# Kernel tuning notes

Hardware: AMD Instinct MI355X
Metric: run time of the kernel (lower is better)

The kernel has to match this reference:

```python
import jax, jax.numpy as jnp
import numpy as np

IN_DIM = 1024
EMBED = 1024
HEADS = 16
HEAD_DIM = EMBED // HEADS
MAX_LEN = 401


def _sinusoidal_pe(max_len, d_model):
    pos = np.arange(max_len, dtype=np.float32)[:, None]
    div = np.exp(np.arange(0, d_model, 2, dtype=np.float32) * (-np.log(10000.0) / d_model))
    pe = np.zeros((max_len, d_model), dtype=np.float32)
    pe[:, 0::2] = np.sin(pos * div)
    pe[:, 1::2] = np.cos(pos * div)
    return jnp.asarray(pe[None])  # [1, max_len, d]


def setup_inputs() -> dict:
    key = jax.random.key(0)
    ks = jax.random.split(key, 16)
    B, S = 32, 400
    s = 1.0 / np.sqrt(IN_DIM)
    inp = {
        "query": jax.random.normal(ks[0], (B, S, IN_DIM), jnp.float32),
        "key": jax.random.normal(ks[1], (B, S, IN_DIM), jnp.float32),
        "value": jax.random.normal(ks[2], (B, S, IN_DIM), jnp.float32),
        "attn_mask": jnp.zeros((S, S), jnp.float32),
        "pe": _sinusoidal_pe(MAX_LEN, IN_DIM),
        "Wq": jax.random.normal(ks[3], (EMBED, IN_DIM), jnp.float32) * s,
        "bq": jax.random.normal(ks[4], (EMBED,), jnp.float32) * s,
        "Wk": jax.random.normal(ks[5], (EMBED, IN_DIM), jnp.float32) * s,
        "bk": jax.random.normal(ks[6], (EMBED,), jnp.float32) * s,
        "Wv": jax.random.normal(ks[7], (EMBED, IN_DIM), jnp.float32) * s,
        "bv": jax.random.normal(ks[8], (EMBED,), jnp.float32) * s,
        "Wp": jax.random.normal(ks[9], (EMBED, IN_DIM), jnp.float32) * s,
        "bp": jax.random.normal(ks[10], (EMBED,), jnp.float32) * s,
        "Wo": jax.random.normal(ks[11], (IN_DIM, EMBED), jnp.float32) / np.sqrt(EMBED),
        "bo": jax.random.normal(ks[12], (IN_DIM,), jnp.float32) / np.sqrt(EMBED),
        "gates": jax.random.normal(ks[13], (1,), jnp.float32),
    }
    return inp


def reference(query, key, value, attn_mask, pe, Wq, bq, Wk, bk, Wv, bv, Wp, bp, Wo, bo, gates):
    B, Sq, _ = query.shape
    Sk = key.shape[1]
    H, D = HEADS, HEAD_DIM

    pos_q = pe[:, :Sq] @ Wp.T + bp   # [1, Sq, E]
    pos_k = pe[:, :Sk] @ Wp.T + bp   # [1, Sk, E]

    q = (query @ Wq.T + bq + pos_q).reshape(B, Sq, H, D).transpose(0, 2, 1, 3)
    k = (key @ Wk.T + bk + pos_k).reshape(B, Sk, H, D).transpose(0, 2, 1, 3)
    v = (value @ Wv.T + bv + pos_k).reshape(B, Sk, H, D).transpose(0, 2, 1, 3)

    scores = jnp.einsum('bhqd,bhkd->bhqk', q, k) / jnp.sqrt(jnp.float32(D))
    scores = scores + attn_mask[None, None]  # additive mask broadcast over batch/heads
    attn = jax.nn.softmax(scores, axis=-1)   # dropout p=0.0 -> identity

    out = jnp.einsum('bhqk,bhkd->bhqd', attn, v)
    out = out.transpose(0, 2, 1, 3).reshape(B, Sq, H * D)
    return (out @ Wo.T + bo) * gates
```

## Files before the change

### kernel.cpp

```cpp
#include <hip/hip_runtime.h>

typedef __bf16 bf16;
typedef __bf16 bf16x8 __attribute__((ext_vector_type(8)));
typedef __bf16 bf16x4 __attribute__((ext_vector_type(4)));
typedef float f32x4 __attribute__((ext_vector_type(4)));

#define MFMA(a, b, c) __builtin_amdgcn_mfma_f32_16x16x32_bf16(a, b, c, 0, 0, 0)

__device__ __forceinline__ void g2l16(void* lds, const void* g) {
  __builtin_amdgcn_global_load_lds(
      (const __attribute__((address_space(1))) void*)g,
      (__attribute__((address_space(3))) void*)lds, 16, 0, 0);
}

__global__ void cvt_all(
    const float* __restrict__ Wq, const float* __restrict__ Wk, const float* __restrict__ Wv,
    const float* __restrict__ Wo, const float* __restrict__ Wp, const float* __restrict__ pe,
    const float* __restrict__ Xq, const float* __restrict__ Xk, const float* __restrict__ Xv,
    bf16* __restrict__ wqb, bf16* __restrict__ wkb, bf16* __restrict__ wvb,
    bf16* __restrict__ wob, bf16* __restrict__ wpb, bf16* __restrict__ peb,
    bf16* __restrict__ xqb, bf16* __restrict__ xkb, bf16* __restrict__ xvb) {
  int b = blockIdx.x;
  const float* s;
  bf16* d;
  int lb;
  if (b < 5120) {
    int t = b >> 10;
    lb = b & 1023;
    s = (t == 0) ? Wq : (t == 1) ? Wk : (t == 2) ? Wv : (t == 3) ? Wo : Wp;
    d = (t == 0) ? wqb : (t == 1) ? wkb : (t == 2) ? wvb : (t == 3) ? wob : wpb;
  } else if (b < 5520) {
    lb = b - 5120;
    s = pe;
    d = peb;
  } else {
    int bb = b - 5520;
    int t = bb / 12800;
    lb = bb - t * 12800;
    s = (t == 0) ? Xq : (t == 1) ? Xk : Xv;
    d = (t == 0) ? xqb : (t == 1) ? xkb : xvb;
  }
  int i = lb * 256 + threadIdx.x;
  f32x4 v = *(const f32x4*)(s + (size_t)i * 4);
  bf16x4 o;
  o[0] = (bf16)v[0]; o[1] = (bf16)v[1]; o[2] = (bf16)v[2]; o[3] = (bf16)v[3];
  *(bf16x4*)(d + (size_t)i * 4) = o;
}

__global__ __launch_bounds__(256) void gemm_pos(
    const bf16* __restrict__ peb, const bf16* __restrict__ Wpb,
    const float* __restrict__ bp, const float* __restrict__ bq,
    const float* __restrict__ bk, const float* __restrict__ bv,
    bf16* __restrict__ posq, bf16* __restrict__ posk, bf16* __restrict__ posv) {
  __shared__ bf16 smA[128 * 32];
  __shared__ bf16 smB[128 * 32];
  const int mbase = blockIdx.y * 128;
  const int nbase = blockIdx.x * 128;
  const int tid = threadIdx.x;
  const int lane = tid & 63, w = tid >> 6;
  const int wm = (w >> 1) * 64, wn = (w & 1) * 64;
  const int lrow = lane & 15, kg = lane >> 4;
  const f32x4 fz = {0.f, 0.f, 0.f, 0.f};
  f32x4 acc[4][4];
#pragma unroll
  for (int i = 0; i < 4; ++i)
#pragma unroll
    for (int j = 0; j < 4; ++j) acc[i][j] = fz;

  for (int k0 = 0; k0 < 1024; k0 += 32) {
    __syncthreads();
#pragma unroll
    for (int it = 0; it < 2; ++it) {
      int j = it * 256 + tid;
      int r = j >> 2, cl = j & 3;
      int c = cl ^ ((r >> 1) & 3);
      if (mbase + r < 400)
        g2l16(smA + j * 8, peb + (mbase + r) * 1024 + k0 + c * 8);
      else {
        uint4 zz = make_uint4(0, 0, 0, 0);
        *(uint4*)(smA + j * 8) = zz;
      }
    }
#pragma unroll
    for (int it = 0; it < 2; ++it) {
      int j = it * 256 + tid;
      int r = j >> 2, cl = j & 3;
      int c = cl ^ ((r >> 1) & 3);
      g2l16(smB + j * 8, Wpb + (nbase + r) * 1024 + k0 + c * 8);
    }
    __syncthreads();
    bf16x8 af[4], bfr[4];
#pragma unroll
    for (int mt = 0; mt < 4; ++mt) {
      int r = wm + mt * 16 + lrow;
      int ch = kg ^ ((r >> 1) & 3);
      af[mt] = *(const bf16x8*)(smA + r * 32 + ch * 8);
    }
#pragma unroll
    for (int nt = 0; nt < 4; ++nt) {
      int r = wn + nt * 16 + lrow;
      int ch = kg ^ ((r >> 1) & 3);
      bfr[nt] = *(const bf16x8*)(smB + r * 32 + ch * 8);
    }
#pragma unroll
    for (int nt = 0; nt < 4; ++nt)
#pragma unroll
      for (int mt = 0; mt < 4; ++mt)
        acc[mt][nt] = MFMA(af[mt], bfr[nt], acc[mt][nt]);
  }
#pragma unroll
  for (int mt = 0; mt < 4; ++mt)
#pragma unroll
    for (int rg = 0; rg < 4; ++rg) {
      int m = mbase + wm + mt * 16 + kg * 4 + rg;
      if (m < 400) {
#pragma unroll
        for (int nt = 0; nt < 4; ++nt) {
          int n = nbase + wn + nt * 16 + lrow;
          float base = acc[mt][nt][rg] + bp[n];
          posq[m * 1024 + n] = (bf16)(base + bq[n]);
          posk[m * 1024 + n] = (bf16)(base + bk[n]);
          posv[m * 1024 + n] = (bf16)(base + bv[n]);
        }
      }
    }
}

__global__ __launch_bounds__(512, 4) void gemm_qkv(
    const bf16* __restrict__ Xqb, const bf16* __restrict__ Xkb, const bf16* __restrict__ Xvb,
    const bf16* __restrict__ Wqb, const bf16* __restrict__ Wkb, const bf16* __restrict__ Wvb,
    const bf16* __restrict__ posq, const bf16* __restrict__ posk, const bf16* __restrict__ posv,
    bf16* __restrict__ qb, bf16* __restrict__ kbuf, bf16* __restrict__ vt) {
  const int lid = blockIdx.x;
  const int mI = ((lid >> 6) << 3) + (lid & 7);
  const int nI = (lid >> 3) & 7;
  if (mI >= 100) return;
  __shared__ bf16 sm[16384];
  bf16* smA = sm;
  bf16* smB = sm + 8192;
  const int z = blockIdx.y;
  const bf16* X = (z == 0) ? Xqb : (z == 1) ? Xkb : Xvb;
  const bf16* W = (z == 0) ? Wqb : (z == 1) ? Wkb : Wvb;
  const bf16* posz = (z == 0) ? posq : (z == 1) ? posk : posv;
  const int mbase = mI * 128;
  const int nbase = nI * 128;
  const int tid = threadIdx.x;
  const int lane = tid & 63, w = tid >> 6;
  const int wm = (w >> 1) * 32, wn = (w & 1) * 64;
  const int lrow = lane & 15, kg = lane >> 4;
  const f32x4 fz = {0.f, 0.f, 0.f, 0.f};
  f32x4 acc[2][4];
#pragma unroll
  for (int i = 0; i < 2; ++i)
#pragma unroll
    for (int j = 0; j < 4; ++j) acc[i][j] = fz;

  for (int k0 = 0; k0 < 1024; k0 += 64) {
    __syncthreads();
#pragma unroll
    for (int it = 0; it < 2; ++it) {
      int j = it * 512 + tid;
      int r = j >> 3, cl = j & 7;
      g2l16(smA + j * 8, X + (size_t)(mbase + r) * 1024 + k0 + (cl ^ (r & 7)) * 8);
    }
#pragma unroll
    for (int it = 0; it < 2; ++it) {
      int j = it * 512 + tid;
      int r = j >> 3, cl = j & 7;
      g2l16(smB + j * 8, W + (size_t)(nbase + r) * 1024 + k0 + (cl ^ (r & 7)) * 8);
    }
    __syncthreads();
#pragma unroll
    for (int ks = 0; ks < 2; ++ks) {
      bf16x8 af[2], bfr[4];
#pragma unroll
      for (int mt = 0; mt < 2; ++mt) {
        int r = wm + mt * 16 + lrow;
        af[mt] = *(const bf16x8*)(smA + r * 64 + ((ks * 4 + kg) ^ (r & 7)) * 8);
      }
#pragma unroll
      for (int nt = 0; nt < 4; ++nt) {
        int r = wn + nt * 16 + lrow;
        bfr[nt] = *(const bf16x8*)(smB + r * 64 + ((ks * 4 + kg) ^ (r & 7)) * 8);
      }
#pragma unroll
      for (int nt = 0; nt < 4; ++nt)
#pragma unroll
        for (int mt = 0; mt < 2; ++mt)
          acc[mt][nt] = MFMA(af[mt], bfr[nt], acc[mt][nt]);
    }
  }

  if (z < 2) {
    bf16* dst = (z == 0) ? qb : kbuf;
#pragma unroll
    for (int mt = 0; mt < 2; ++mt)
#pragma unroll
      for (int rg = 0; rg < 4; ++rg) {
        int m = mbase + wm + mt * 16 + kg * 4 + rg;
        int bI = m / 400;
        int s = m - bI * 400;
#pragma unroll
        for (int nt = 0; nt < 4; ++nt) {
          int n = nbase + wn + nt * 16 + lrow;
          float v = acc[mt][nt][rg] + (float)posz[s * 1024 + n];
          int h = n >> 6, d = n & 63;
          dst[((size_t)(bI * 16 + h) * 400 + s) * 64 + d] = (bf16)v;
        }
      }
  } else {
    __syncthreads();
    bf16* T = sm;
#pragma unroll
    for (int nt = 0; nt < 4; ++nt) {
      int n = wn + nt * 16 + lrow;
      int ng = nbase + n;
#pragma unroll
      for (int mt = 0; mt < 2; ++mt) {
        int m0 = wm + mt * 16 + kg * 4;
        bf16x4 v4;
#pragma unroll
        for (int rg = 0; rg < 4; ++rg) {
          int m = mbase + m0 + rg;
          int bI = m / 400;
          int s = m - bI * 400;
          v4[rg] = (bf16)(acc[mt][nt][rg] + (float)posz[s * 1024 + ng]);
        }
        int chk = m0 >> 3;
        int st = chk ^ (n & 15);
        *(bf16x4*)(T + n * 128 + st * 8 + (m0 & 7)) = v4;
      }
    }
    __syncthreads();
#pragma unroll
    for (int p = 0; p < 4; ++p) {
      int n = p * 32 + (tid >> 4);
      int chk = tid & 15;
      bf16x8 row = *(const bf16x8*)(T + n * 128 + (chk ^ (n & 15)) * 8);
      int ng = nbase + n;
      int h = ng >> 6, d = ng & 63;
      int m = mbase + chk * 8;
      int bI = m / 400;
      int s = m - bI * 400;
      *(bf16x8*)(vt + ((size_t)(bI * 16 + h) * 64 + d) * 400 + s) = row;
    }
  }
}

__global__ __launch_bounds__(512, 4) void attn_kernel(
    const bf16* __restrict__ qg, const bf16* __restrict__ kg_,
    const bf16* __restrict__ vg, const float* __restrict__ mask,
    bf16* __restrict__ ao) {
  const int lid = blockIdx.x;
  const int qt = (lid >> 3) & 3;
  const int bh = ((lid >> 5) << 3) + (lid & 7);
  __shared__ bf16 smQ[128 * 64];
  __shared__ bf16 smK[128 * 64];
  __shared__ bf16 smV[64 * 128];
  __shared__ bf16 smP[128 * 128];
  const int qbase = qt * 128;
  const int tid = threadIdx.x;
  const int lane = tid & 63;
  const int w = tid >> 6;
  const int lrow = lane & 15, kg = lane >> 4;
  const bf16* Qg = qg + bh * 25600;
  const bf16* Kg = kg_ + bh * 25600;
  const bf16* Vg = vg + bh * 25600;

#pragma unroll
  for (int it = 0; it < 2; ++it) {
    int j = it * 512 + tid;
    int r = j >> 3, cl = j & 7;
    int c = cl ^ (r & 7);
    int s = qbase + r;
    uint4 val = make_uint4(0, 0, 0, 0);
    if (s < 400) val = *(const uint4*)(Qg + s * 64 + c * 8);
    *(uint4*)(smQ + j * 8) = val;
  }

  const f32x4 fz = {0.f, 0.f, 0.f, 0.f};
  f32x4 o[4];
#pragma unroll
  for (int i = 0; i < 4; ++i) o[i] = fz;
  float m_run[4], l_run[4];
#pragma unroll
  for (int i = 0; i < 4; ++i) { m_run[i] = -1e30f; l_run[i] = 0.f; }

  for (int kt = 0; kt < 4; ++kt) {
#pragma unroll
    for (int it = 0; it < 2; ++it) {
      int j = it * 512 + tid;
      int r = j >> 3, cl = j & 7;
      int c = cl ^ (r & 7);
      int s = kt * 128 + r;
      uint4 val = make_uint4(0, 0, 0, 0);
      if (s < 400) val = *(const uint4*)(Kg + s * 64 + c * 8);
      *(uint4*)(smK + j * 8) = val;
    }
#pragma unroll
    for (int it = 0; it < 2; ++it) {
      int j = it * 512 + tid;
      int r = j >> 4, cl = j & 15;
      int c = cl ^ (r & 15);
      int s0 = kt * 128 + c * 8;
      uint4 val = make_uint4(0, 0, 0, 0);
      if (s0 < 400) val = *(const uint4*)(Vg + r * 400 + s0);
      *(uint4*)(smV + j * 8) = val;
    }
    __syncthreads();

    f32x4 sc[8];
#pragma unroll
    for (int nt = 0; nt < 8; ++nt) sc[nt] = fz;
#pragma unroll
    for (int ks = 0; ks < 2; ++ks) {
      int rq = w * 16 + lrow;
      int chq = (ks * 4 + kg) ^ (rq & 7);
      bf16x8 aq = *(const bf16x8*)(smQ + rq * 64 + chq * 8);
#pragma unroll
      for (int nt = 0; nt < 8; ++nt) {
        int rk = nt * 16 + lrow;
        int chk = (ks * 4 + kg) ^ (rk & 7);
        bf16x8 bk8 = *(const bf16x8*)(smK + rk * 64 + chk * 8);
        sc[nt] = MFMA(aq, bk8, sc[nt]);
      }
    }
    float alpha[4];
#pragma unroll
    for (int rg = 0; rg < 4; ++rg) {
      int qs = qbase + w * 16 + kg * 4 + rg;
      float rmax = -1e30f;
#pragma unroll
      for (int nt = 0; nt < 8; ++nt) {
        int ksi = kt * 128 + nt * 16 + lrow;
        float v = sc[nt][rg] * 0.125f;
        v += (ksi < 400) ? ((qs < 400) ? mask[qs * 400 + ksi] : 0.f) : -1e30f;
        sc[nt][rg] = v;
        rmax = fmaxf(rmax, v);
      }
#pragma unroll
      for (int off = 1; off < 16; off <<= 1)
        rmax = fmaxf(rmax, __shfl_xor(rmax, off, 64));
      float mn = fmaxf(m_run[rg], rmax);
      alpha[rg] = __expf(m_run[rg] - mn);
      m_run[rg] = mn;
      float rsum = 0.f;
#pragma unroll
      for (int nt = 0; nt < 8; ++nt) {
        float p = __expf(sc[nt][rg] - mn);
        sc[nt][rg] = p;
        rsum += p;
      }
#pragma unroll
      for (int off = 1; off < 16; off <<= 1)
        rsum += __shfl_xor(rsum, off, 64);
      l_run[rg] = l_run[rg] * alpha[rg] + rsum;
    }
#pragma unroll
    for (int nt2 = 0; nt2 < 4; ++nt2)
#pragma unroll
      for (int rg = 0; rg < 4; ++rg) o[nt2][rg] *= alpha[rg];
#pragma unroll
    for (int nt = 0; nt < 8; ++nt)
#pragma unroll
      for (int rg = 0; rg < 4; ++rg) {
        int row = w * 16 + kg * 4 + rg;
        int col = nt * 16 + lrow;
        int ch = (col >> 3) ^ (row & 15);
        smP[row * 128 + ch * 8 + (col & 7)] = (bf16)sc[nt][rg];
      }
    __syncthreads();
#pragma unroll
    for (int ks2 = 0; ks2 < 4; ++ks2) {
      int rp = w * 16 + lrow;
      int chp = (ks2 * 4 + kg) ^ (rp & 15);
      bf16x8 ap = *(const bf16x8*)(smP + rp * 128 + chp * 8);
#pragma unroll
      for (int nt2 = 0; nt2 < 4; ++nt2) {
        int rv = nt2 * 16 + lrow;
        int chv = (ks2 * 4 + kg) ^ (rv & 15);
        bf16x8 bv8 = *(const bf16x8*)(smV + rv * 128 + chv * 8);
        o[nt2] = MFMA(ap, bv8, o[nt2]);
      }
    }
    __syncthreads();
  }
  const int b = bh >> 4, h = bh & 15;
#pragma unroll
  for (int rg = 0; rg < 4; ++rg) {
    int qs = qbase + w * 16 + kg * 4 + rg;
    if (qs < 400) {
      float inv = 1.f / l_run[rg];
#pragma unroll
      for (int nt2 = 0; nt2 < 4; ++nt2) {
        ao[(b * 400 + qs) * 1024 + h * 64 + nt2 * 16 + lrow] =
            (bf16)(o[nt2][rg] * inv);
      }
    }
  }
}

__global__ __launch_bounds__(512, 4) void gemm_out(
    const bf16* __restrict__ aop, const bf16* __restrict__ Wob,
    const float* __restrict__ bo, const float* __restrict__ gates,
    float* __restrict__ out) {
  const int lid = blockIdx.x;
  const int mI = ((lid >> 6) << 3) + (lid & 7);
  const int nI = (lid >> 3) & 7;
  if (mI >= 100) return;
  __shared__ bf16 sm[16384];
  bf16* smA = sm;
  bf16* smB = sm + 8192;
  const int mbase = mI * 128;
  const int nbase = nI * 128;
  const int tid = threadIdx.x;
  const int lane = tid & 63, w = tid >> 6;
  const int wm = (w >> 1) * 32, wn = (w & 1) * 64;
  const int lrow = lane & 15, kg = lane >> 4;
  const float g = gates[0];
  const f32x4 fz = {0.f, 0.f, 0.f, 0.f};
  f32x4 acc[2][4];
#pragma unroll
  for (int i = 0; i < 2; ++i)
#pragma unroll
    for (int j = 0; j < 4; ++j) acc[i][j] = fz;

  for (int k0 = 0; k0 < 1024; k0 += 64) {
    __syncthreads();
#pragma unroll
    for (int it = 0; it < 2; ++it) {
      int j = it * 512 + tid;
      int r = j >> 3, cl = j & 7;
      g2l16(smA + j * 8, aop + (size_t)(mbase + r) * 1024 + k0 + (cl ^ (r & 7)) * 8);
    }
#pragma unroll
    for (int it = 0; it < 2; ++it) {
      int j = it * 512 + tid;
      int r = j >> 3, cl = j & 7;
      g2l16(smB + j * 8, Wob + (size_t)(nbase + r) * 1024 + k0 + (cl ^ (r & 7)) * 8);
    }
    __syncthreads();
#pragma unroll
    for (int ks = 0; ks < 2; ++ks) {
      bf16x8 af[2], bfr[4];
#pragma unroll
      for (int mt = 0; mt < 2; ++mt) {
        int r = wm + mt * 16 + lrow;
        af[mt] = *(const bf16x8*)(smA + r * 64 + ((ks * 4 + kg) ^ (r & 7)) * 8);
      }
#pragma unroll
      for (int nt = 0; nt < 4; ++nt) {
        int r = wn + nt * 16 + lrow;
        bfr[nt] = *(const bf16x8*)(smB + r * 64 + ((ks * 4 + kg) ^ (r & 7)) * 8);
      }
#pragma unroll
      for (int nt = 0; nt < 4; ++nt)
#pragma unroll
        for (int mt = 0; mt < 2; ++mt)
          acc[mt][nt] = MFMA(af[mt], bfr[nt], acc[mt][nt]);
    }
  }
#pragma unroll
  for (int mt = 0; mt < 2; ++mt)
#pragma unroll
    for (int rg = 0; rg < 4; ++rg) {
      int m = mbase + wm + mt * 16 + kg * 4 + rg;
#pragma unroll
      for (int nt = 0; nt < 4; ++nt) {
        int n = nbase + wn + nt * 16 + lrow;
        out[(size_t)m * 1024 + n] = (acc[mt][nt][rg] + bo[n]) * g;
      }
    }
}

extern "C" void kernel_launch(void* const* d_in, const int* in_sizes, int n_in,
                              void* d_out, int out_size, void* d_ws, size_t ws_size,
                              hipStream_t stream) {
  const float* query = (const float*)d_in[0];
  const float* key   = (const float*)d_in[1];
  const float* value = (const float*)d_in[2];
  const float* mask  = (const float*)d_in[3];
  const float* pe    = (const float*)d_in[4];
  const float* Wq = (const float*)d_in[5];
  const float* bq = (const float*)d_in[6];
  const float* Wk = (const float*)d_in[7];
  const float* bk = (const float*)d_in[8];
  const float* Wv = (const float*)d_in[9];
  const float* bv = (const float*)d_in[10];
  const float* Wp = (const float*)d_in[11];
  const float* bp = (const float*)d_in[12];
  const float* Wo = (const float*)d_in[13];
  const float* bo = (const float*)d_in[14];
  const float* gates = (const float*)d_in[15];
  float* out = (float*)d_out;

  char* base = (char*)d_ws;
  size_t off = 0;
  bf16* wq_b = (bf16*)(base + off); off += 2097152;
  bf16* wk_b = (bf16*)(base + off); off += 2097152;
  bf16* wv_b = (bf16*)(base + off); off += 2097152;
  bf16* wo_b = (bf16*)(base + off); off += 2097152;
  bf16* wp_b = (bf16*)(base + off); off += 2097152;
  bf16* pe_b = (bf16*)(base + off); off += 819200;
  bf16* posq = (bf16*)(base + off); off += 819200;
  bf16* posk = (bf16*)(base + off); off += 819200;
  bf16* posv = (bf16*)(base + off); off += 819200;
  bf16* qb = (bf16*)(base + off); off += 26214400;
  bf16* kb = (bf16*)(base + off); off += 26214400;
  bf16* vt = (bf16*)(base + off); off += 26214400;
  bf16* ao = (bf16*)(base + off); off += 26214400;
  bf16* xq_b = ao;
  bf16* xk_b = (bf16*)d_out;
  bf16* xv_b = (bf16*)d_out + 13107200;
  (void)ws_size; (void)in_sizes; (void)n_in; (void)out_size;

  cvt_all<<<43920, 256, 0, stream>>>(Wq, Wk, Wv, Wo, Wp, pe,
                                     query, key, value,
                                     wq_b, wk_b, wv_b, wo_b, wp_b, pe_b,
                                     xq_b, xk_b, xv_b);
  gemm_pos<<<dim3(8, 4), 256, 0, stream>>>(pe_b, wp_b, bp, bq, bk, bv,
                                           posq, posk, posv);
  gemm_qkv<<<dim3(832, 3), 512, 0, stream>>>(xq_b, xk_b, xv_b,
                                             wq_b, wk_b, wv_b,
                                             posq, posk, posv, qb, kb, vt);
  attn_kernel<<<2048, 512, 0, stream>>>(qb, kb, vt, mask, ao);
  gemm_out<<<832, 512, 0, stream>>>(ao, wo_b, bo, gates, out);
}
```

Before: 524.1 us.

## Prefetch next K/V tile into registers and raise MFMA wave priority in attention

The attention kernel now loads the next key/value tile from global memory into registers while the current tile is being computed, then writes it to LDS at the start of the next iteration. This hides global load latency behind the QK and softmax work. It also wraps the MFMA loops with s_setprio and splits the mask/bounds handling so full tiles skip the per-element bounds checks, using an fma for scale plus mask. The cost is extra register pressure from holding the prefetched tiles, which could lower occupancy.

```diff
diff --git a/kernel.cpp b/kernel.cpp
--- a/kernel.cpp
+++ b/kernel.cpp
@@ -278,6 +278,22 @@
     *(uint4*)(smQ + j * 8) = val;
   }
 
+  uint4 rk[2], rv[2];
+#pragma unroll
+  for (int it = 0; it < 2; ++it) {
+    int j = it * 512 + tid;
+    int r = j >> 3, cl = j & 7;
+    int c = cl ^ (r & 7);
+    rk[it] = *(const uint4*)(Kg + r * 64 + c * 8);
+  }
+#pragma unroll
+  for (int it = 0; it < 2; ++it) {
+    int j = it * 512 + tid;
+    int r = j >> 4, cl = j & 15;
+    int c = cl ^ (r & 15);
+    rv[it] = *(const uint4*)(Vg + r * 400 + c * 8);
+  }
+
   const f32x4 fz = {0.f, 0.f, 0.f, 0.f};
   f32x4 o[4];
 #pragma unroll
@@ -290,28 +306,41 @@
 #pragma unroll
     for (int it = 0; it < 2; ++it) {
       int j = it * 512 + tid;
-      int r = j >> 3, cl = j & 7;
-      int c = cl ^ (r & 7);
-      int s = kt * 128 + r;
-      uint4 val = make_uint4(0, 0, 0, 0);
-      if (s < 400) val = *(const uint4*)(Kg + s * 64 + c * 8);
-      *(uint4*)(smK + j * 8) = val;
+      *(uint4*)(smK + j * 8) = rk[it];
     }
 #pragma unroll
     for (int it = 0; it < 2; ++it) {
       int j = it * 512 + tid;
-      int r = j >> 4, cl = j & 15;
-      int c = cl ^ (r & 15);
-      int s0 = kt * 128 + c * 8;
-      uint4 val = make_uint4(0, 0, 0, 0);
-      if (s0 < 400) val = *(const uint4*)(Vg + r * 400 + s0);
-      *(uint4*)(smV + j * 8) = val;
+      *(uint4*)(smV + j * 8) = rv[it];
+    }
+    if (kt < 3) {
+#pragma unroll
+      for (int it = 0; it < 2; ++it) {
+        int j = it * 512 + tid;
+        int r = j >> 3, cl = j & 7;
+        int c = cl ^ (r & 7);
+        int s = (kt + 1) * 128 + r;
+        uint4 val = make_uint4(0, 0, 0, 0);
+        if (s < 400) val = *(const uint4*)(Kg + s * 64 + c * 8);
+        rk[it] = val;
+      }
+#pragma unroll
+      for (int it = 0; it < 2; ++it) {
+        int j = it * 512 + tid;
+        int r = j >> 4, cl = j & 15;
+        int c = cl ^ (r & 15);
+        int s0 = (kt + 1) * 128 + c * 8;
+        uint4 val = make_uint4(0, 0, 0, 0);
+        if (s0 < 400) val = *(const uint4*)(Vg + r * 400 + s0);
+        rv[it] = val;
+      }
     }
     __syncthreads();
 
     f32x4 sc[8];
 #pragma unroll
     for (int nt = 0; nt < 8; ++nt) sc[nt] = fz;
+    __builtin_amdgcn_s_setprio(1);
 #pragma unroll
     for (int ks = 0; ks < 2; ++ks) {
       int rq = w * 16 + lrow;
@@ -319,24 +348,35 @@
       bf16x8 aq = *(const bf16x8*)(smQ + rq * 64 + chq * 8);
 #pragma unroll
       for (int nt = 0; nt < 8; ++nt) {
-        int rk = nt * 16 + lrow;
-        int chk = (ks * 4 + kg) ^ (rk & 7);
-        bf16x8 bk8 = *(const bf16x8*)(smK + rk * 64 + chk * 8);
+        int rk2 = nt * 16 + lrow;
+        int chk = (ks * 4 + kg) ^ (rk2 & 7);
+        bf16x8 bk8 = *(const bf16x8*)(smK + rk2 * 64 + chk * 8);
         sc[nt] = MFMA(aq, bk8, sc[nt]);
       }
     }
+    __builtin_amdgcn_s_setprio(0);
     float alpha[4];
 #pragma unroll
     for (int rg = 0; rg < 4; ++rg) {
       int qs = qbase + w * 16 + kg * 4 + rg;
+      const float* mrow = mask + (size_t)((qs < 400) ? qs : 399) * 400;
       float rmax = -1e30f;
-#pragma unroll
-      for (int nt = 0; nt < 8; ++nt) {
-        int ksi = kt * 128 + nt * 16 + lrow;
-        float v = sc[nt][rg] * 0.125f;
-        v += (ksi < 400) ? ((qs < 400) ? mask[qs * 400 + ksi] : 0.f) : -1e30f;
-        sc[nt][rg] = v;
-        rmax = fmaxf(rmax, v);
+      if (kt < 3) {
+#pragma unroll
+        for (int nt = 0; nt < 8; ++nt) {
+          int ksi = kt * 128 + nt * 16 + lrow;
+          float v = fmaf(sc[nt][rg], 0.125f, mrow[ksi]);
+          sc[nt][rg] = v;
+          rmax = fmaxf(rmax, v);
+        }
+      } else {
+#pragma unroll
+        for (int nt = 0; nt < 8; ++nt) {
+          int ksi = 384 + nt * 16 + lrow;
+          float v = (ksi < 400) ? fmaf(sc[nt][rg], 0.125f, mrow[ksi]) : -1e30f;
+          sc[nt][rg] = v;
+          rmax = fmaxf(rmax, v);
+        }
       }
 #pragma unroll
       for (int off = 1; off < 16; off <<= 1)
@@ -370,6 +410,7 @@
         smP[row * 128 + ch * 8 + (col & 7)] = (bf16)sc[nt][rg];
       }
     __syncthreads();
+    __builtin_amdgcn_s_setprio(1);
 #pragma unroll
     for (int ks2 = 0; ks2 < 4; ++ks2) {
       int rp = w * 16 + lrow;
@@ -377,12 +418,13 @@
       bf16x8 ap = *(const bf16x8*)(smP + rp * 128 + chp * 8);
 #pragma unroll
       for (int nt2 = 0; nt2 < 4; ++nt2) {
-        int rv = nt2 * 16 + lrow;
-        int chv = (ks2 * 4 + kg) ^ (rv & 15);
-        bf16x8 bv8 = *(const bf16x8*)(smV + rv * 128 + chv * 8);
+        int rv2 = nt2 * 16 + lrow;
+        int chv = (ks2 * 4 + kg) ^ (rv2 & 15);
+        bf16x8 bv8 = *(const bf16x8*)(smV + rv2 * 128 + chv * 8);
         o[nt2] = MFMA(ap, bv8, o[nt2]);
       }
     }
+    __builtin_amdgcn_s_setprio(0);
     __syncthreads();
   }
   const int b = bh >> 4, h = bh & 15;
```

Measured after the change: 678.9 us. +29.5%, slower.
